# Performance work log

Hardware: AMD Instinct MI355X
Metric: run time of the kernel (lower is better)

## Reference

```python
import jax, jax.numpy as jnp
import numpy as np

EPS = 1e-5


def setup_inputs() -> dict:
    key = jax.random.key(0)
    k0, k1, k2, k3 = jax.random.split(key, 4)
    B, C, H, W = 64, 128, 64, 64
    x = jax.random.normal(k0, (B, C, H, W), dtype=jnp.float32)
    w = jax.random.normal(k1, (C, C, 1), dtype=jnp.float32) * 0.05  # conv1d kernel_size=1 weight
    b = jax.random.normal(k2, (C,), dtype=jnp.float32) * 0.05       # conv1d bias
    s = jax.random.normal(k3, (1, C, 1), dtype=jnp.float32)         # learned per-channel gate logits
    offset = jnp.ones((1,), dtype=jnp.float32) * 8.0                 # module inits offset to 8
    return {"x": x, "w": w, "b": b, "s": s, "offset": offset}


def reference(x, w, b, s, offset):
    B, C, H, W = x.shape
    HW = H * W
    # Checkerboard mask: mask[c, l] = (c + l) % 2  (even channel -> [0,1,0,1,...])
    c_idx = jnp.arange(C)
    l_idx = jnp.arange(HW)
    mask = ((c_idx[:, None] + l_idx[None, :]) % 2).astype(x.dtype)  # (C, HW)

    x_flat = x.reshape(B, C, HW)
    x_masked = x_flat * mask                                         # (B, C, HW)
    # 1x1 conv1d: pointwise channel mix + bias
    z = jnp.einsum('oc,bcl->bol', w[:, :, 0], x_masked) + b[None, :, None]
    pool = z.mean(axis=1)                                            # avgpool over channels -> (B, HW)
    g = jax.nn.sigmoid(pool + offset) + EPS                          # (B, HW)
    s_sig = jax.nn.sigmoid(s[0, :, 0]) + EPS                         # (C,)

    attn_mask = (1.0 - mask)[None] * g[:, None, :] + mask[None] * s_sig[None, :, None]  # (B,C,HW)
    out = x * attn_mask.reshape(B, C, H, W)

    logdet = (C // 2) * jnp.sum(jnp.log(g), axis=-1)                 # (B,)
    logdet = logdet + B * jnp.sum(jnp.log(s_sig)[:, None] * mask)    # scalar broadcast over batch
    return out, logdet
```

## Files before the change

kernel.cpp:

```cpp
#include <hip/hip_runtime.h>
#include <hip/hip_bf16.h>
#include <math.h>


#define EPS 1e-5f
#define NC 128
#define NHW 4096
#define NB 64
#define LT 64
#define NLT (NHW / LT)


__global__ __launch_bounds__(128) void prep_kernel(const float* __restrict__ w,
                                                   const float* __restrict__ bias,
                                                   const float* __restrict__ s,
                                                   float* __restrict__ ws) {
    __shared__ float red[NC];
    const int c = threadIdx.x;
    float acc = 0.f;
    for (int o = 0; o < NC; ++o) acc += w[o * NC + c];
    ws[c] = acc * (1.f / NC);
    const float sv = s[c];
    const float ssig = 1.f / (1.f + expf(-sv)) + EPS;
    ws[NC + c] = ssig;

    red[c] = bias[c];
    __syncthreads();
    if (c == 0) {
        double sb = 0.0;
        for (int i = 0; i < NC; ++i) sb += (double)red[i];
        ws[256] = (float)(sb / NC);
    }
    __syncthreads();
    red[c] = logf(ssig);
    __syncthreads();
    if (c == 0) {
        double sl = 0.0;
        for (int i = 0; i < NC; ++i) sl += (double)red[i];
        ws[257] = (float)((double)NB * (double)(NHW / 2) * sl);
    }
}

__global__ __launch_bounds__(256) void main_kernel(const float* __restrict__ x,
                                                   const float* __restrict__ ws,
                                                   const float* __restrict__ offp,
                                                   float* __restrict__ out,
                                                   float* __restrict__ partials) {
    __shared__ float xs[NC][LT];
    __shared__ float pp[4][LT];
    __shared__ float gsh[LT];

    const int tid = threadIdx.x;
    const int lt  = blockIdx.x;
    const int b   = blockIdx.y;
    const int l0  = lt * LT;
    const size_t xbase = (size_t)b * (NC * NHW) + l0;

#pragma unroll
    for (int it = 0; it < 8; ++it) {
        const int idx = it * 256 + tid;
        const int c = idx >> 4;
        const int j = idx & 15;
        const float4 v = *reinterpret_cast<const float4*>(x + xbase + (size_t)c * NHW + j * 4);
        *reinterpret_cast<float4*>(&xs[c][j * 4]) = v;
    }
    __syncthreads();

    const int l = tid & 63;
    const int q = tid >> 6;
    {
        float acc = 0.f;
#pragma unroll
        for (int cc = 0; cc < 32; ++cc) {
            const int c = q * 32 + cc;
            const float m = (float)((c + l) & 1);
            acc += m * ws[c] * xs[c][l];
        }
        pp[q][l] = acc;
    }
    __syncthreads();

    float g = 0.f;
    if (tid < 64) {
        const float pool = pp[0][l] + pp[1][l] + pp[2][l] + pp[3][l] + ws[256];
        const float t = pool + offp[0];
        g = 1.f / (1.f + __expf(-t)) + EPS;
        gsh[l] = g;
    }
    __syncthreads();

    if (tid < 64) {
        float lg = __logf(g);
#pragma unroll
        for (int off = 32; off > 0; off >>= 1) lg += __shfl_down(lg, off);
        if (tid == 0) partials[b * gridDim.x + lt] = lg;
    }

    const float* __restrict__ ssig = ws + NC;
#pragma unroll
    for (int it = 0; it < 8; ++it) {
        const int idx = it * 256 + tid;
        const int c = idx >> 4;
        const int j = idx & 15;
        const float sc = ssig[c];
        const float4 v = *reinterpret_cast<const float4*>(&xs[c][j * 4]);
        float4 o;
        const float g0 = gsh[j * 4 + 0];
        const float g1 = gsh[j * 4 + 1];
        const float g2 = gsh[j * 4 + 2];
        const float g3 = gsh[j * 4 + 3];
        if (c & 1) {
            o.x = v.x * sc;  o.y = v.y * g1;  o.z = v.z * sc;  o.w = v.w * g3;
        } else {
            o.x = v.x * g0;  o.y = v.y * sc;  o.z = v.z * g2;  o.w = v.w * sc;
        }
        *reinterpret_cast<float4*>(out + xbase + (size_t)c * NHW + j * 4) = o;
    }
}

__global__ __launch_bounds__(64) void fin_kernel(const float* __restrict__ partials,
                                                 const float* __restrict__ ws,
                                                 float* __restrict__ logdet,
                                                 int nlt) {
    const int b = blockIdx.x;
    const int t = threadIdx.x;
    float v = (t < nlt) ? partials[b * nlt + t] : 0.f;
#pragma unroll
    for (int off = 32; off > 0; off >>= 1) v += __shfl_down(v, off);
    if (t == 0) logdet[b] = 64.f * v + ws[257];
}

extern "C" void kernel_launch(void* const* d_in, const int* in_sizes, int n_in,
                              void* d_out, int out_size, void* d_ws, size_t ws_size,
                              hipStream_t stream) {
    const float* x    = (const float*)d_in[0];
    const float* w    = (const float*)d_in[1];
    const float* bias = (const float*)d_in[2];
    const float* s    = (const float*)d_in[3];
    const float* offp = (const float*)d_in[4];

    float* out = (float*)d_out;
    float* logdet = out + (size_t)NB * NC * NHW;

    float* ws = (float*)d_ws;
    float* partials = ws + 512;

    const int nlt = NHW / LT;

    prep_kernel<<<1, 128, 0, stream>>>(w, bias, s, ws);
    main_kernel<<<dim3(nlt, NB), 256, 0, stream>>>(x, ws, offp, out, partials);
    fin_kernel<<<NB, 64, 0, stream>>>(partials, ws, logdet, nlt);
}
```

Baseline: 56.28 us.

## Keep x tile in registers and reduce channels with shuffles instead of LDS

Each thread now loads 8 channels by 4 columns of x straight into registers and keeps them there for the output pass. The 32KB shared-memory staging of the x tile is removed. The masked channel dot product is reduced with cross-lane xor shuffles plus a small shared array of float4 partials, which drops two barriers and the per-element mask arithmetic. Lower LDS use may allow higher occupancy, at the cost of more registers per thread.

```diff
diff --git a/kernel.cpp b/kernel.cpp
--- a/kernel.cpp
+++ b/kernel.cpp
@@ -46,75 +46,74 @@
                                                    const float* __restrict__ offp,
                                                    float* __restrict__ out,
                                                    float* __restrict__ partials) {
-    __shared__ float xs[NC][LT];
-    __shared__ float pp[4][LT];
-    __shared__ float gsh[LT];
+    __shared__ float4 pp[4][16];
 
-    const int tid = threadIdx.x;
-    const int lt  = blockIdx.x;
-    const int b   = blockIdx.y;
-    const int l0  = lt * LT;
-    const size_t xbase = (size_t)b * (NC * NHW) + l0;
+    const int tid  = threadIdx.x;
+    const int j    = tid & 15;
+    const int cg   = tid >> 4;
+    const int wave = tid >> 6;
+    const int lane = tid & 63;
+
+    const int lt = blockIdx.x;
+    const int b  = blockIdx.y;
+    const int l0 = lt * LT;
+
+    const size_t base = (size_t)b * (NC * NHW) + (size_t)(cg * 8) * NHW + l0 + j * 4;
+    const float* __restrict__ xp = x + base;
+
+    float4 v[8];
+#pragma unroll
+    for (int k = 0; k < 8; ++k)
+        v[k] = *reinterpret_cast<const float4*>(xp + (size_t)k * NHW);
+
+    float4 acc = make_float4(0.f, 0.f, 0.f, 0.f);
+#pragma unroll
+    for (int k = 0; k < 8; ++k) {
+        const int c = cg * 8 + k;
+        const float wb = ws[c];
+        if (c & 1) { acc.x += wb * v[k].x; acc.z += wb * v[k].z; }
+        else       { acc.y += wb * v[k].y; acc.w += wb * v[k].w; }
+    }
 
 #pragma unroll
-    for (int it = 0; it < 8; ++it) {
-        const int idx = it * 256 + tid;
-        const int c = idx >> 4;
-        const int j = idx & 15;
-        const float4 v = *reinterpret_cast<const float4*>(x + xbase + (size_t)c * NHW + j * 4);
-        *reinterpret_cast<float4*>(&xs[c][j * 4]) = v;
+    for (int off = 16; off <= 32; off <<= 1) {
+        acc.x += __shfl_xor(acc.x, off);
+        acc.y += __shfl_xor(acc.y, off);
+        acc.z += __shfl_xor(acc.z, off);
+        acc.w += __shfl_xor(acc.w, off);
     }
+    if (lane < 16) pp[wave][j] = acc;
     __syncthreads();
 
-    const int l = tid & 63;
-    const int q = tid >> 6;
-    {
-        float acc = 0.f;
+    const float4 p0 = pp[0][j], p1 = pp[1][j], p2 = pp[2][j], p3 = pp[3][j];
+    const float cst = ws[256] + offp[0];
+    float4 g;
+    g.x = 1.f / (1.f + __expf(-(p0.x + p1.x + p2.x + p3.x + cst))) + EPS;
+    g.y = 1.f / (1.f + __expf(-(p0.y + p1.y + p2.y + p3.y + cst))) + EPS;
+    g.z = 1.f / (1.f + __expf(-(p0.z + p1.z + p2.z + p3.z + cst))) + EPS;
+    g.w = 1.f / (1.f + __expf(-(p0.w + p1.w + p2.w + p3.w + cst))) + EPS;
+
+    if (wave == 0) {
+        float slg = (lane < 16)
+                  ? (__logf(g.x) + __logf(g.y) + __logf(g.z) + __logf(g.w))
+                  : 0.f;
 #pragma unroll
-        for (int cc = 0; cc < 32; ++cc) {
-            const int c = q * 32 + cc;
-            const float m = (float)((c + l) & 1);
-            acc += m * ws[c] * xs[c][l];
-        }
-        pp[q][l] = acc;
-    }
-    __syncthreads();
-
-    float g = 0.f;
-    if (tid < 64) {
-        const float pool = pp[0][l] + pp[1][l] + pp[2][l] + pp[3][l] + ws[256];
-        const float t = pool + offp[0];
-        g = 1.f / (1.f + __expf(-t)) + EPS;
-        gsh[l] = g;
-    }
-    __syncthreads();
-
-    if (tid < 64) {
-        float lg = __logf(g);
-#pragma unroll
-        for (int off = 32; off > 0; off >>= 1) lg += __shfl_down(lg, off);
-        if (tid == 0) partials[b * gridDim.x + lt] = lg;
+        for (int off = 32; off > 0; off >>= 1) slg += __shfl_down(slg, off);
+        if (lane == 0) partials[b * gridDim.x + lt] = slg;
     }
 
     const float* __restrict__ ssig = ws + NC;
+    float* __restrict__ op = out + base;
 #pragma unroll
-    for (int it = 0; it < 8; ++it) {
-        const int idx = it * 256 + tid;
-        const int c = idx >> 4;
-        const int j = idx & 15;
+    for (int k = 0; k < 8; ++k) {
+        const int c = cg * 8 + k;
         const float sc = ssig[c];
-        const float4 v = *reinterpret_cast<const float4*>(&xs[c][j * 4]);
         float4 o;
-        const float g0 = gsh[j * 4 + 0];
-        const float g1 = gsh[j * 4 + 1];
-        const float g2 = gsh[j * 4 + 2];
-        const float g3 = gsh[j * 4 + 3];
-        if (c & 1) {
-            o.x = v.x * sc;  o.y = v.y * g1;  o.z = v.z * sc;  o.w = v.w * g3;
-        } else {
-            o.x = v.x * g0;  o.y = v.y * sc;  o.z = v.z * g2;  o.w = v.w * sc;
-        }
-        *reinterpret_cast<float4*>(out + xbase + (size_t)c * NHW + j * 4) = o;
+        if (c & 1) { o.x = v[k].x * sc;  o.y = v[k].y * g.y;
+                     o.z = v[k].z * sc;  o.w = v[k].w * g.w; }
+        else       { o.x = v[k].x * g.x; o.y = v[k].y * sc;
+                     o.z = v[k].z * g.z; o.w = v[k].w * sc; }
+        *reinterpret_cast<float4*>(op + (size_t)k * NHW) = o;
     }
 }
 
```

Result: no change. 55.68 us (-1.1%).
